# Performance work log

Hardware: AMD Instinct MI355X
Metric: run time of the kernel (lower is better)

Reference implementation:

```python
import jax, jax.numpy as jnp
import numpy as np

B, S, N = 8, 4096, 512
K_DIM, HEADS, WS = 512, 8, 128
HD = K_DIM // HEADS


def setup_inputs() -> dict:
    key = jax.random.key(0)
    ks = jax.random.split(key, 9)
    sc = 0.02
    return {
        "inputs": jax.random.normal(ks[0], (B, S, N), dtype=jnp.float32),
        "Wq": jax.random.normal(ks[1], (K_DIM, N), dtype=jnp.float32) * sc,
        "bq": jax.random.normal(ks[2], (K_DIM,), dtype=jnp.float32) * sc,
        "Wk": jax.random.normal(ks[3], (K_DIM, N), dtype=jnp.float32) * sc,
        "bk": jax.random.normal(ks[4], (K_DIM,), dtype=jnp.float32) * sc,
        "Wv": jax.random.normal(ks[5], (K_DIM, N), dtype=jnp.float32) * sc,
        "bv": jax.random.normal(ks[6], (K_DIM,), dtype=jnp.float32) * sc,
        "Wp": jax.random.normal(ks[7], (N, K_DIM), dtype=jnp.float32) * sc,
        "bp": jax.random.normal(ks[8], (N,), dtype=jnp.float32) * sc,
    }


def reference(inputs, Wq, bq, Wk, bk, Wv, bv, Wp, bp):
    b, s, n = inputs.shape
    nw = s // WS  # number of windows per sequence
    # QKV projections (torch Linear: x @ W.T + b)
    q = inputs @ Wq.T + bq  # [B,S,K]
    k = inputs @ Wk.T + bk
    v = inputs @ Wv.T + bv

    def to_windows(t):
        # [B,S,K] -> [B*nw, H, WS, HD]
        t = t.reshape(b * nw, WS, HEADS, HD)
        return t.transpose(0, 2, 1, 3)

    q, k, v = to_windows(q), to_windows(k), to_windows(v)
    scale = HD ** (-0.5)
    # windowed attention: [BW,H,WS,WS]
    score = jnp.einsum('whqd,whkd->whqk', q, k) * scale
    attn = jax.nn.softmax(score, axis=-1)  # dropout is identity in eval
    out = jnp.einsum('whqk,whkd->whqd', attn, v)  # [BW,H,WS,HD]
    out = out.transpose(0, 2, 1, 3).reshape(b, s, K_DIM)  # window reverse
    out = out @ Wp.T + bp  # [B,S,N]
    return out
```

## Files before the change

kernel.cpp:

```cpp
#include <hip/hip_runtime.h>
#include <hip/hip_bf16.h>
#include <stdint.h>


typedef __bf16 bf16;
typedef __bf16 bf16x8 __attribute__((ext_vector_type(8)));
typedef __bf16 bf16x4 __attribute__((ext_vector_type(4)));
typedef __bf16 bf16x2 __attribute__((ext_vector_type(2)));
typedef float  f32x4  __attribute__((ext_vector_type(4)));

#define DEV static __device__ __forceinline__

DEV void gld_lds16(const bf16* g, bf16* l) {
  __builtin_amdgcn_global_load_lds(
      (__attribute__((address_space(1))) void*)(g),
      (__attribute__((address_space(3))) void*)(l), 16, 0, 0);
}

__global__ void cast_all(const float* __restrict__ x,
                         const float* __restrict__ Wq, const float* __restrict__ Wk,
                         const float* __restrict__ Wv, const float* __restrict__ Wp,
                         bf16* __restrict__ xb, bf16* __restrict__ wb) {
  int i = blockIdx.x * blockDim.x + threadIdx.x;
  const float* src;
  bf16* dst;
  if (i < 4194304) {
    src = x + i * 4;
    dst = xb + i * 4;
  } else {
    int e = (i - 4194304) * 4;
    int off;
    const float* w;
    if (e < 786432) {
      int seg = e >> 18;
      off = e & 262143;
      w = (seg == 0) ? Wq : ((seg == 1) ? Wk : Wv);
    } else {
      off = e - 786432;
      w = Wp;
    }
    src = w + off;
    dst = wb + e;
  }
  float4 v = *(const float4*)src;
  bf16x4 o;
  o[0] = (bf16)v.x; o[1] = (bf16)v.y; o[2] = (bf16)v.z; o[3] = (bf16)v.w;
  *(bf16x4*)dst = o;
}

template <bool BF16OUT, int NTILES>
__global__ __launch_bounds__(512, 2)
void gemm256(const bf16* __restrict__ A, const bf16* __restrict__ B,
             const float* __restrict__ bias0, const float* __restrict__ bias1,
             const float* __restrict__ bias2, void* __restrict__ Cout) {
  constexpr int Ntot = NTILES * 256;
  __shared__ __align__(16) bf16 smem[2][2][256 * 64];

  const int tid = threadIdx.x;
  const int wave = tid >> 6, lane = tid & 63;
  const int wm = wave >> 2, wn = wave & 3;
  const int lane15 = lane & 15, kq = lane >> 4;
  const int srow = lane >> 3, sg = (lane & 7) ^ srow;

  const int nb = gridDim.x;
  const int j = blockIdx.x;
  const int l = (j & 7) * (nb >> 3) + (j >> 3);
  const long row0 = (long)(l / NTILES) * 256;
  const long col0 = (long)(l % NTILES) * 256;

  f32x4 acc[8][4] = {};
  bf16x8 af[4][2], bfr[2][2];

#define STAGE(T, BUF)                                                          \
  {                                                                            \
    const long kb_ = (long)(T) * 64;                                           \
    _Pragma("unroll") for (int i_ = 0; i_ < 4; ++i_) {                         \
      const int r0_ = wave * 32 + i_ * 8;                                      \
      gld_lds16(A + (row0 + r0_ + srow) * 512 + kb_ + sg * 8,                  \
                &smem[BUF][0][r0_ * 64]);                                      \
      gld_lds16(B + (col0 + r0_ + srow) * 512 + kb_ + sg * 8,                  \
                &smem[BUF][1][r0_ * 64]);                                      \
    }                                                                          \
  }

#define READ_A(QM, BUF)                                                        \
  {                                                                            \
    _Pragma("unroll") for (int mt_ = 0; mt_ < 4; ++mt_) {                      \
      const int r_ = wm * 128 + (QM) * 64 + mt_ * 16 + lane15;                 \
      const bf16* p_ = &smem[BUF][0][r_ * 64];                                 \
      _Pragma("unroll") for (int ks_ = 0; ks_ < 2; ++ks_) {                    \
        const int c_ = (ks_ * 4 + kq) ^ (r_ & 7);                              \
        af[mt_][ks_] = *(const bf16x8*)(p_ + c_ * 8);                          \
      }                                                                        \
    }                                                                          \
  }

#define READ_B(QN, BUF)                                                        \
  {                                                                            \
    _Pragma("unroll") for (int nt_ = 0; nt_ < 2; ++nt_) {                      \
      const int r_ = wn * 64 + (QN) * 32 + nt_ * 16 + lane15;                  \
      const bf16* p_ = &smem[BUF][1][r_ * 64];                                 \
      _Pragma("unroll") for (int ks_ = 0; ks_ < 2; ++ks_) {                    \
        const int c_ = (ks_ * 4 + kq) ^ (r_ & 7);                              \
        bfr[nt_][ks_] = *(const bf16x8*)(p_ + c_ * 8);                         \
      }                                                                        \
    }                                                                          \
  }

#define MMA_Q(QM, QN)                                                          \
  {                                                                            \
    __builtin_amdgcn_s_setprio(1);                                             \
    _Pragma("unroll") for (int mt_ = 0; mt_ < 4; ++mt_)                        \
    _Pragma("unroll") for (int nt_ = 0; nt_ < 2; ++nt_)                        \
    _Pragma("unroll") for (int ks_ = 0; ks_ < 2; ++ks_)                        \
      acc[(QM) * 4 + mt_][(QN) * 2 + nt_] =                                    \
          __builtin_amdgcn_mfma_f32_16x16x32_bf16(                             \
              af[mt_][ks_], bfr[nt_][ks_],                                     \
              acc[(QM) * 4 + mt_][(QN) * 2 + nt_], 0, 0, 0);                   \
    __builtin_amdgcn_s_setprio(0);                                             \
  }

  STAGE(0, 0);
  STAGE(1, 1);
  asm volatile("s_waitcnt vmcnt(8)" ::: "memory");
  __builtin_amdgcn_s_barrier();

  for (int kt = 0; kt < 8; ++kt) {
    const int cur = kt & 1;
    READ_A(0, cur); READ_B(0, cur);
    __builtin_amdgcn_s_barrier();
    MMA_Q(0, 0);
    __builtin_amdgcn_s_barrier();
    READ_B(1, cur);
    __builtin_amdgcn_s_barrier();
    MMA_Q(0, 1);
    __builtin_amdgcn_s_barrier();
    READ_A(1, cur);
    __builtin_amdgcn_s_barrier();
    MMA_Q(1, 1);
    __builtin_amdgcn_s_barrier();
    READ_B(0, cur);
    __builtin_amdgcn_s_barrier();
    MMA_Q(1, 0);
    __builtin_amdgcn_s_barrier();

    if (kt + 2 < 8) {
      STAGE(kt + 2, cur);
      asm volatile("s_waitcnt vmcnt(8)" ::: "memory");
      __builtin_amdgcn_s_barrier();
    } else if (kt + 1 < 8) {
      asm volatile("s_waitcnt vmcnt(0)" ::: "memory");
      __builtin_amdgcn_s_barrier();
    }
  }

#undef STAGE
#undef READ_A
#undef READ_B
#undef MMA_Q

  const long crow = row0 + wm * 128;
  const long ccol = col0 + wn * 64;
  for (int m = 0; m < 8; ++m) {
    for (int n = 0; n < 4; ++n) {
      const long col = ccol + n * 16 + lane15;
      const float* bsel;
      if (NTILES == 6) {
        const int seg = (int)(col >> 9);
        bsel = (seg == 0) ? bias0 : ((seg == 1) ? bias1 : bias2);
      } else {
        bsel = bias0;
      }
      const float bias = bsel[col & 511];
      const long row = crow + m * 16 + kq * 4;
      for (int g = 0; g < 4; ++g) {
        const float v = acc[m][n][g] + bias;
        if (BF16OUT) ((bf16*)Cout)[(row + g) * Ntot + col] = (bf16)v;
        else         ((float*)Cout)[(row + g) * Ntot + col] = v;
      }
    }
  }
}

__global__ __launch_bounds__(512, 4)
void attn_win(const bf16* __restrict__ QKV, bf16* __restrict__ Out) {
  __shared__ __align__(16) char smem[49152];
  bf16* Qs = (bf16*)smem;
  bf16* Ks = Qs + 128 * 64;
  bf16* Ps = (bf16*)smem;
  bf16* Vt = (bf16*)(smem + 32768);

  const int tid = threadIdx.x;
  const int wave = tid >> 6, lane = tid & 63;
  const int lane15 = lane & 15, quad = lane >> 4;
  const int win = blockIdx.x >> 3, head = blockIdx.x & 7;

  const bf16* Qg = QKV + (size_t)win * 128 * 1536 + head * 64;
  const bf16* Kg = Qg + 512;
  const bf16* Vg = Qg + 1024;

  {
    const int srow = lane >> 3;
    const int sg = (lane & 7) ^ srow;
    for (int i = 0; i < 2; ++i) {
      int r0 = (wave * 2 + i) * 8;
      gld_lds16(Qg + (size_t)(r0 + srow) * 1536 + sg * 8, Qs + r0 * 64 + lane * 8);
      gld_lds16(Kg + (size_t)(r0 + srow) * 1536 + sg * 8, Ks + r0 * 64 + lane * 8);
    }
  }
  {
    int tp = tid >> 3;
    int d0 = (tid & 7) * 8;
    bf16x8 v0 = *(const bf16x8*)(Vg + (size_t)(2 * tp) * 1536 + d0);
    bf16x8 v1 = *(const bf16x8*)(Vg + (size_t)(2 * tp + 1) * 1536 + d0);
    int gt = tp >> 2, po = tp & 3;
    for (int j = 0; j < 8; ++j) {
      int d = d0 + j;
      int p = gt ^ ((d >> 3) ^ (d & 7));
      bf16x2 pr;
      pr[0] = v0[j]; pr[1] = v1[j];
      *(bf16x2*)(Vt + d * 128 + p * 8 + po * 2) = pr;
    }
  }
  __syncthreads();

  f32x4 accs[8] = {};
  {
    bf16x8 aq[2];
    for (int s = 0; s < 2; ++s) {
      int row = wave * 16 + lane15;
      aq[s] = *(const bf16x8*)(Qs + row * 64 + (((s * 4 + quad) ^ (lane15 & 7)) * 8));
    }
    for (int c = 0; c < 8; ++c) {
      int row = c * 16 + lane15;
      for (int s = 0; s < 2; ++s) {
        bf16x8 bk = *(const bf16x8*)(Ks + row * 64 + (((s * 4 + quad) ^ (lane15 & 7)) * 8));
        accs[c] = __builtin_amdgcn_mfma_f32_16x16x32_bf16(aq[s], bk, accs[c], 0, 0, 0);
      }
    }
  }
  __syncthreads();

  const float scale = 0.125f;
  for (int g = 0; g < 4; ++g) {
    float sum = 0.f;
    for (int c = 0; c < 8; ++c) {
      float e = __expf(accs[c][g] * scale);
      accs[c][g] = e;
      sum += e;
    }
    for (int mk = 1; mk <= 8; mk <<= 1) sum += __shfl_xor(sum, mk, 64);
    float inv = 1.0f / sum;
    int prow = wave * 16 + quad * 4 + g;
    int rsw = prow & 7;
    for (int c = 0; c < 8; ++c) {
      int col = c * 16 + lane15;
      int p = (col >> 3) ^ rsw;
      Ps[prow * 128 + p * 8 + (col & 7)] = (bf16)(accs[c][g] * inv);
    }
  }
  __syncthreads();

  f32x4 acco[4] = {};
  for (int kk = 0; kk < 4; ++kk) {
    int arow = wave * 16 + lane15;
    int pa = (kk * 4 + quad) ^ (arow & 7);
    bf16x8 a = *(const bf16x8*)(Ps + arow * 128 + pa * 8);
    for (int c = 0; c < 4; ++c) {
      int d = c * 16 + lane15;
      int p = (kk * 4 + quad) ^ ((d >> 3) ^ (d & 7));
      bf16x8 b = *(const bf16x8*)(Vt + d * 128 + p * 8);
      acco[c] = __builtin_amdgcn_mfma_f32_16x16x32_bf16(a, b, acco[c], 0, 0, 0);
    }
  }

  bf16* Og = Out + (size_t)win * 128 * 512 + head * 64;
  {
    int row = wave * 16 + quad * 4;
    for (int c = 0; c < 4; ++c) {
      int col = c * 16 + lane15;
      for (int g = 0; g < 4; ++g)
        Og[(size_t)(row + g) * 512 + col] = (bf16)acco[c][g];
    }
  }
}

extern "C" void kernel_launch(void* const* d_in, const int* in_sizes, int n_in,
                              void* d_out, int out_size, void* d_ws, size_t ws_size,
                              hipStream_t stream) {
  const float* x  = (const float*)d_in[0];
  const float* Wq = (const float*)d_in[1];
  const float* bq = (const float*)d_in[2];
  const float* Wk = (const float*)d_in[3];
  const float* bk = (const float*)d_in[4];
  const float* Wv = (const float*)d_in[5];
  const float* bv = (const float*)d_in[6];
  const float* Wp = (const float*)d_in[7];
  const float* bp = (const float*)d_in[8];

  bf16* Xb    = (bf16*)d_ws;
  bf16* Wqkvb = Xb + 16777216;
  bf16* Wpb   = Wqkvb + 786432;
  bf16* QKVb  = Wpb + 262144;
  bf16* AttnB = QKVb + 50331648;

  cast_all<<<17408, 256, 0, stream>>>(x, Wq, Wk, Wv, Wp, Xb, Wqkvb);
  gemm256<true, 6><<<768, 512, 0, stream>>>(Xb, Wqkvb, bq, bk, bv, QKVb);
  attn_win<<<2048, 512, 0, stream>>>(QKVb, AttnB);
  gemm256<false, 2><<<256, 512, 0, stream>>>(AttnB, Wpb, bp, bp, bp, d_out);
}
```

Measured before the change: 252.5 us.

## Chain QKV GEMM over column tiles per block and retile output projection

The QKV projection GEMM now has each of 256 blocks walk three 256-wide column tiles in sequence with one continuous prefetch pipeline, so there is exactly one wave of blocks on the GPU. Each tile's result is written out with bias before the next tile starts. The output projection switches to a new 128x128-tile kernel using 32x32x16 MFMA with 1024 blocks, which raises parallelism compared with the previous 256 large blocks. The trade-offs are a longer serial chain per block in the first GEMM and a simpler, unpipelined load loop with more sync points in the second.

```diff
diff --git a/kernel.cpp b/kernel.cpp
--- a/kernel.cpp
+++ b/kernel.cpp
@@ -8,6 +8,7 @@
 typedef __bf16 bf16x4 __attribute__((ext_vector_type(4)));
 typedef __bf16 bf16x2 __attribute__((ext_vector_type(2)));
 typedef float  f32x4  __attribute__((ext_vector_type(4)));
+typedef float  f32x16 __attribute__((ext_vector_type(16)));
 
 #define DEV static __device__ __forceinline__
 
@@ -48,12 +49,14 @@
   *(bf16x4*)dst = o;
 }
 
-template <bool BF16OUT, int NTILES>
+template <int NTILES, int CHAIN>
 __global__ __launch_bounds__(512, 2)
-void gemm256(const bf16* __restrict__ A, const bf16* __restrict__ B,
-             const float* __restrict__ bias0, const float* __restrict__ bias1,
-             const float* __restrict__ bias2, void* __restrict__ Cout) {
+void gemm256c(const bf16* __restrict__ A, const bf16* __restrict__ B,
+              const float* __restrict__ bias0, const float* __restrict__ bias1,
+              const float* __restrict__ bias2, bf16* __restrict__ Cout) {
   constexpr int Ntot = NTILES * 256;
+  constexpr int CG = NTILES / CHAIN;
+  constexpr int NK = CHAIN * 8;
   __shared__ __align__(16) bf16 smem[2][2][256 * 64];
 
   const int tid = threadIdx.x;
@@ -62,23 +65,22 @@
   const int lane15 = lane & 15, kq = lane >> 4;
   const int srow = lane >> 3, sg = (lane & 7) ^ srow;
 
-  const int nb = gridDim.x;
-  const int j = blockIdx.x;
-  const int l = (j & 7) * (nb >> 3) + (j >> 3);
-  const long row0 = (long)(l / NTILES) * 256;
-  const long col0 = (long)(l % NTILES) * 256;
+  const int b = blockIdx.x;
+  const long row0 = (long)(b / CG) * 256;
+  const int cgbase = (b % CG) * CHAIN;
 
   f32x4 acc[8][4] = {};
   bf16x8 af[4][2], bfr[2][2];
 
 #define STAGE(T, BUF)                                                          \
   {                                                                            \
-    const long kb_ = (long)(T) * 64;                                           \
+    const long colt_ = (long)(cgbase + ((T) >> 3)) * 256;                      \
+    const long kb_ = (long)((T) & 7) * 64;                                     \
     _Pragma("unroll") for (int i_ = 0; i_ < 4; ++i_) {                         \
       const int r0_ = wave * 32 + i_ * 8;                                      \
       gld_lds16(A + (row0 + r0_ + srow) * 512 + kb_ + sg * 8,                  \
                 &smem[BUF][0][r0_ * 64]);                                      \
-      gld_lds16(B + (col0 + r0_ + srow) * 512 + kb_ + sg * 8,                  \
+      gld_lds16(B + (colt_ + r0_ + srow) * 512 + kb_ + sg * 8,                 \
                 &smem[BUF][1][r0_ * 64]);                                      \
     }                                                                          \
   }
@@ -125,32 +127,54 @@
   asm volatile("s_waitcnt vmcnt(8)" ::: "memory");
   __builtin_amdgcn_s_barrier();
 
-  for (int kt = 0; kt < 8; ++kt) {
-    const int cur = kt & 1;
-    READ_A(0, cur); READ_B(0, cur);
-    __builtin_amdgcn_s_barrier();
-    MMA_Q(0, 0);
-    __builtin_amdgcn_s_barrier();
-    READ_B(1, cur);
-    __builtin_amdgcn_s_barrier();
-    MMA_Q(0, 1);
-    __builtin_amdgcn_s_barrier();
-    READ_A(1, cur);
-    __builtin_amdgcn_s_barrier();
-    MMA_Q(1, 1);
-    __builtin_amdgcn_s_barrier();
-    READ_B(0, cur);
-    __builtin_amdgcn_s_barrier();
-    MMA_Q(1, 0);
-    __builtin_amdgcn_s_barrier();
-
-    if (kt + 2 < 8) {
-      STAGE(kt + 2, cur);
-      asm volatile("s_waitcnt vmcnt(8)" ::: "memory");
-      __builtin_amdgcn_s_barrier();
-    } else if (kt + 1 < 8) {
-      asm volatile("s_waitcnt vmcnt(0)" ::: "memory");
-      __builtin_amdgcn_s_barrier();
+  for (int t = 0; t < CHAIN; ++t) {
+    for (int kt = 0; kt < 8; ++kt) {
+      const int kk = t * 8 + kt;
+      const int cur = kk & 1;
+      READ_A(0, cur); READ_B(0, cur);
+      __builtin_amdgcn_s_barrier();
+      MMA_Q(0, 0);
+      __builtin_amdgcn_s_barrier();
+      READ_B(1, cur);
+      __builtin_amdgcn_s_barrier();
+      MMA_Q(0, 1);
+      __builtin_amdgcn_s_barrier();
+      READ_A(1, cur);
+      __builtin_amdgcn_s_barrier();
+      MMA_Q(1, 1);
+      __builtin_amdgcn_s_barrier();
+      READ_B(0, cur);
+      __builtin_amdgcn_s_barrier();
+      MMA_Q(1, 0);
+      __builtin_amdgcn_s_barrier();
+
+      if (kk + 2 < NK) {
+        STAGE(kk + 2, cur);
+        asm volatile("s_waitcnt vmcnt(8)" ::: "memory");
+        __builtin_amdgcn_s_barrier();
+      } else if (kk + 1 < NK) {
+        asm volatile("s_waitcnt vmcnt(0)" ::: "memory");
+        __builtin_amdgcn_s_barrier();
+      }
+    }
+
+    {
+      const long crow = row0 + wm * 128;
+      const long ccol = (long)(cgbase + t) * 256 + wn * 64;
+      for (int m = 0; m < 8; ++m) {
+        for (int n = 0; n < 4; ++n) {
+          const long col = ccol + n * 16 + lane15;
+          const int seg = (int)(col >> 9);
+          const float* bsel = (seg == 0) ? bias0 : ((seg == 1) ? bias1 : bias2);
+          const float bias = bsel[col & 511];
+          const long row = crow + m * 16 + kq * 4;
+          for (int g = 0; g < 4; ++g) {
+            const float v = acc[m][n][g] + bias;
+            Cout[(row + g) * Ntot + col] = (bf16)v;
+          }
+          acc[m][n] = (f32x4){0.f, 0.f, 0.f, 0.f};
+        }
+      }
     }
   }
 
@@ -158,25 +182,67 @@
 #undef READ_A
 #undef READ_B
 #undef MMA_Q
-
-  const long crow = row0 + wm * 128;
-  const long ccol = col0 + wn * 64;
-  for (int m = 0; m < 8; ++m) {
-    for (int n = 0; n < 4; ++n) {
-      const long col = ccol + n * 16 + lane15;
-      const float* bsel;
-      if (NTILES == 6) {
-        const int seg = (int)(col >> 9);
-        bsel = (seg == 0) ? bias0 : ((seg == 1) ? bias1 : bias2);
-      } else {
-        bsel = bias0;
-      }
-      const float bias = bsel[col & 511];
-      const long row = crow + m * 16 + kq * 4;
-      for (int g = 0; g < 4; ++g) {
-        const float v = acc[m][n][g] + bias;
-        if (BF16OUT) ((bf16*)Cout)[(row + g) * Ntot + col] = (bf16)v;
-        else         ((float*)Cout)[(row + g) * Ntot + col] = v;
+}
+
+template <bool BF16OUT, int NCOL>
+__global__ __launch_bounds__(256, 4)
+void gemm_bt(const bf16* __restrict__ A, const bf16* __restrict__ B,
+             const float* __restrict__ bias0, void* __restrict__ Cout) {
+  constexpr int Ntot = NCOL * 128;
+  __shared__ bf16 As[128 * 64];
+  __shared__ bf16 Bs[128 * 64];
+  const int tid = threadIdx.x;
+  const int wave = tid >> 6, lane = tid & 63;
+  const int wm = wave >> 1, wn = wave & 1;
+  const int lane31 = lane & 31, khalf = lane >> 5;
+
+  const int nb = gridDim.x;
+  const int j = blockIdx.x;
+  const int l = (j & 7) * (nb >> 3) + (j >> 3);
+  const long row0 = (long)(l / NCOL) * 128;
+  const long col0 = (long)(l % NCOL) * 128;
+
+  f32x16 acc[2][2] = {};
+
+  const int srow = lane >> 3;
+  const int sg = (lane & 7) ^ srow;
+
+  for (int k0 = 0; k0 < 512; k0 += 64) {
+    __syncthreads();
+    for (int i = 0; i < 4; ++i) {
+      int r0 = (wave * 4 + i) * 8;
+      gld_lds16(A + (row0 + r0 + srow) * 512 + k0 + sg * 8, As + r0 * 64 + lane * 8);
+      gld_lds16(B + (col0 + r0 + srow) * 512 + k0 + sg * 8, Bs + r0 * 64 + lane * 8);
+    }
+    __syncthreads();
+    for (int s = 0; s < 4; ++s) {
+      bf16x8 af[2], bfr[2];
+      for (int r = 0; r < 2; ++r) {
+        int row = wm * 64 + r * 32 + lane31;
+        int ph = (s * 2 + khalf) ^ (row & 7);
+        af[r] = *(const bf16x8*)(As + row * 64 + ph * 8);
+      }
+      for (int c = 0; c < 2; ++c) {
+        int row = wn * 64 + c * 32 + lane31;
+        int ph = (s * 2 + khalf) ^ (row & 7);
+        bfr[c] = *(const bf16x8*)(Bs + row * 64 + ph * 8);
+      }
+      for (int r = 0; r < 2; ++r)
+        for (int c = 0; c < 2; ++c)
+          acc[r][c] = __builtin_amdgcn_mfma_f32_32x32x16_bf16(af[r], bfr[c], acc[r][c], 0, 0, 0);
+    }
+  }
+
+  for (int r = 0; r < 2; ++r) {
+    for (int c = 0; c < 2; ++c) {
+      long col = col0 + wn * 64 + c * 32 + lane31;
+      float bias = bias0[col & 511];
+      for (int reg = 0; reg < 16; ++reg) {
+        int rr = (reg & 3) + 8 * (reg >> 2) + 4 * khalf;
+        long row = row0 + wm * 64 + r * 32 + rr;
+        float v = acc[r][c][reg] + bias;
+        if (BF16OUT) ((bf16*)Cout)[row * Ntot + col] = (bf16)v;
+        else        ((float*)Cout)[row * Ntot + col] = v;
       }
     }
   }
@@ -305,7 +371,7 @@
   bf16* AttnB = QKVb + 50331648;
 
   cast_all<<<17408, 256, 0, stream>>>(x, Wq, Wk, Wv, Wp, Xb, Wqkvb);
-  gemm256<true, 6><<<768, 512, 0, stream>>>(Xb, Wqkvb, bq, bk, bv, QKVb);
+  gemm256c<6, 3><<<256, 512, 0, stream>>>(Xb, Wqkvb, bq, bk, bv, QKVb);
   attn_win<<<2048, 512, 0, stream>>>(QKVb, AttnB);
-  gemm256<false, 2><<<256, 512, 0, stream>>>(AttnB, Wpb, bp, bp, bp, d_out);
-}
+  gemm_bt<false, 4><<<1024, 256, 0, stream>>>(AttnB, Wpb, bp, d_out);
+}
```

After: 261.2 us. +3.5%, slower.

## Interleave next-tile global loads with LDS reads and MMAs in GEMM main loop

Applied to the files above, without the earlier changes.

The GEMM main loop changes from prefetching two k-tiles ahead in one batch to prefetching one tile ahead, with its global-to-LDS loads split into three chunks placed between the LDS fragment reads of the current tile. Separate A/B fragment registers let the last two MMA quadrants run back to back with fewer barriers, and the MMA loop order now puts k-step outermost. The goal is to hide load latency behind MMA work and cut barrier count. The cost is a shorter prefetch distance and a full vmcnt(0) wait every iteration, which could expose memory latency.

```diff
diff --git a/kernel.cpp b/kernel.cpp
--- a/kernel.cpp
+++ b/kernel.cpp
@@ -50,10 +50,11 @@
 
 template <bool BF16OUT, int NTILES>
 __global__ __launch_bounds__(512, 2)
-void gemm256(const bf16* __restrict__ A, const bf16* __restrict__ B,
-             const float* __restrict__ bias0, const float* __restrict__ bias1,
-             const float* __restrict__ bias2, void* __restrict__ Cout) {
+void gemm256f(const bf16* __restrict__ A, const bf16* __restrict__ B,
+              const float* __restrict__ bias0, const float* __restrict__ bias1,
+              const float* __restrict__ bias2, void* __restrict__ Cout) {
   constexpr int Ntot = NTILES * 256;
+  constexpr int NK = 8;
   __shared__ __align__(16) bf16 smem[2][2][256 * 64];
 
   const int tid = threadIdx.x;
@@ -69,92 +70,88 @@
   const long col0 = (long)(l % NTILES) * 256;
 
   f32x4 acc[8][4] = {};
-  bf16x8 af[4][2], bfr[2][2];
-
-#define STAGE(T, BUF)                                                          \
-  {                                                                            \
-    const long kb_ = (long)(T) * 64;                                           \
-    _Pragma("unroll") for (int i_ = 0; i_ < 4; ++i_) {                         \
-      const int r0_ = wave * 32 + i_ * 8;                                      \
-      gld_lds16(A + (row0 + r0_ + srow) * 512 + kb_ + sg * 8,                  \
-                &smem[BUF][0][r0_ * 64]);                                      \
-      gld_lds16(B + (col0 + r0_ + srow) * 512 + kb_ + sg * 8,                  \
-                &smem[BUF][1][r0_ * 64]);                                      \
-    }                                                                          \
-  }
-
-#define READ_A(QM, BUF)                                                        \
+  bf16x8 af0[4][2], af1[4][2], bq0[2][2], bq1[2][2];
+
+#define STG_A(T, BUF, I)                                                       \
+  gld_lds16(A + (row0 + wave * 32 + (I) * 8 + srow) * 512 + (long)(T) * 64 +   \
+                sg * 8,                                                        \
+            &smem[BUF][0][(wave * 32 + (I) * 8) * 64]);
+#define STG_B(T, BUF, I)                                                       \
+  gld_lds16(B + (col0 + wave * 32 + (I) * 8 + srow) * 512 + (long)(T) * 64 +   \
+                sg * 8,                                                        \
+            &smem[BUF][1][(wave * 32 + (I) * 8) * 64]);
+
+#define READ_A(DST, QM, BUF)                                                   \
   {                                                                            \
     _Pragma("unroll") for (int mt_ = 0; mt_ < 4; ++mt_) {                      \
       const int r_ = wm * 128 + (QM) * 64 + mt_ * 16 + lane15;                 \
       const bf16* p_ = &smem[BUF][0][r_ * 64];                                 \
       _Pragma("unroll") for (int ks_ = 0; ks_ < 2; ++ks_) {                    \
         const int c_ = (ks_ * 4 + kq) ^ (r_ & 7);                              \
-        af[mt_][ks_] = *(const bf16x8*)(p_ + c_ * 8);                          \
+        DST[mt_][ks_] = *(const bf16x8*)(p_ + c_ * 8);                         \
       }                                                                        \
     }                                                                          \
   }
 
-#define READ_B(QN, BUF)                                                        \
+#define READ_B(DST, QN, BUF)                                                   \
   {                                                                            \
     _Pragma("unroll") for (int nt_ = 0; nt_ < 2; ++nt_) {                      \
       const int r_ = wn * 64 + (QN) * 32 + nt_ * 16 + lane15;                  \
       const bf16* p_ = &smem[BUF][1][r_ * 64];                                 \
       _Pragma("unroll") for (int ks_ = 0; ks_ < 2; ++ks_) {                    \
         const int c_ = (ks_ * 4 + kq) ^ (r_ & 7);                              \
-        bfr[nt_][ks_] = *(const bf16x8*)(p_ + c_ * 8);                         \
+        DST[nt_][ks_] = *(const bf16x8*)(p_ + c_ * 8);                         \
       }                                                                        \
     }                                                                          \
   }
 
-#define MMA_Q(QM, QN)                                                          \
+#define MMA_Q(AF, BF, QM, QN)                                                  \
   {                                                                            \
     __builtin_amdgcn_s_setprio(1);                                             \
+    _Pragma("unroll") for (int ks_ = 0; ks_ < 2; ++ks_)                        \
     _Pragma("unroll") for (int mt_ = 0; mt_ < 4; ++mt_)                        \
     _Pragma("unroll") for (int nt_ = 0; nt_ < 2; ++nt_)                        \
-    _Pragma("unroll") for (int ks_ = 0; ks_ < 2; ++ks_)                        \
       acc[(QM) * 4 + mt_][(QN) * 2 + nt_] =                                    \
           __builtin_amdgcn_mfma_f32_16x16x32_bf16(                             \
-              af[mt_][ks_], bfr[nt_][ks_],                                     \
+              AF[mt_][ks_], BF[nt_][ks_],                                      \
               acc[(QM) * 4 + mt_][(QN) * 2 + nt_], 0, 0, 0);                   \
     __builtin_amdgcn_s_setprio(0);                                             \
   }
 
-  STAGE(0, 0);
-  STAGE(1, 1);
-  asm volatile("s_waitcnt vmcnt(8)" ::: "memory");
+  {
+    STG_A(0, 0, 0) STG_A(0, 0, 1) STG_A(0, 0, 2) STG_A(0, 0, 3)
+    STG_B(0, 0, 0) STG_B(0, 0, 1) STG_B(0, 0, 2) STG_B(0, 0, 3)
+  }
+  asm volatile("s_waitcnt vmcnt(0)" ::: "memory");
   __builtin_amdgcn_s_barrier();
 
-  for (int kt = 0; kt < 8; ++kt) {
-    const int cur = kt & 1;
-    READ_A(0, cur); READ_B(0, cur);
-    __builtin_amdgcn_s_barrier();
-    MMA_Q(0, 0);
-    __builtin_amdgcn_s_barrier();
-    READ_B(1, cur);
-    __builtin_amdgcn_s_barrier();
-    MMA_Q(0, 1);
-    __builtin_amdgcn_s_barrier();
-    READ_A(1, cur);
-    __builtin_amdgcn_s_barrier();
-    MMA_Q(1, 1);
-    __builtin_amdgcn_s_barrier();
-    READ_B(0, cur);
-    __builtin_amdgcn_s_barrier();
-    MMA_Q(1, 0);
-    __builtin_amdgcn_s_barrier();
-
-    if (kt + 2 < 8) {
-      STAGE(kt + 2, cur);
-      asm volatile("s_waitcnt vmcnt(8)" ::: "memory");
-      __builtin_amdgcn_s_barrier();
-    } else if (kt + 1 < 8) {
+  for (int kk = 0; kk < NK; ++kk) {
+    const int cur = kk & 1, nxt = cur ^ 1;
+    const bool st = (kk + 1 < NK);
+    READ_A(af0, 0, cur);
+    READ_B(bq0, 0, cur);
+    if (st) { STG_A(kk + 1, nxt, 0) STG_A(kk + 1, nxt, 1) STG_B(kk + 1, nxt, 0) }
+    __builtin_amdgcn_s_barrier();
+    MMA_Q(af0, bq0, 0, 0);
+    __builtin_amdgcn_s_barrier();
+    READ_B(bq1, 1, cur);
+    if (st) { STG_A(kk + 1, nxt, 2) STG_A(kk + 1, nxt, 3) STG_B(kk + 1, nxt, 1) }
+    __builtin_amdgcn_s_barrier();
+    MMA_Q(af0, bq1, 0, 1);
+    __builtin_amdgcn_s_barrier();
+    READ_A(af1, 1, cur);
+    if (st) { STG_B(kk + 1, nxt, 2) STG_B(kk + 1, nxt, 3) }
+    __builtin_amdgcn_s_barrier();
+    MMA_Q(af1, bq1, 1, 1);
+    MMA_Q(af1, bq0, 1, 0);
+    if (st) {
       asm volatile("s_waitcnt vmcnt(0)" ::: "memory");
       __builtin_amdgcn_s_barrier();
     }
   }
 
-#undef STAGE
+#undef STG_A
+#undef STG_B
 #undef READ_A
 #undef READ_B
 #undef MMA_Q
@@ -305,7 +302,7 @@
   bf16* AttnB = QKVb + 50331648;
 
   cast_all<<<17408, 256, 0, stream>>>(x, Wq, Wk, Wv, Wp, Xb, Wqkvb);
-  gemm256<true, 6><<<768, 512, 0, stream>>>(Xb, Wqkvb, bq, bk, bv, QKVb);
+  gemm256f<true, 6><<<768, 512, 0, stream>>>(Xb, Wqkvb, bq, bk, bv, QKVb);
   attn_win<<<2048, 512, 0, stream>>>(QKVb, AttnB);
-  gemm256<false, 2><<<256, 512, 0, stream>>>(AttnB, Wpb, bp, bp, bp, d_out);
-}
+  gemm256f<false, 2><<<256, 512, 0, stream>>>(AttnB, Wpb, bp, bp, bp, d_out);
+}
```

Result: faster. 242.0 us (-4.1%).
